# Performance work log

Hardware: AMD Instinct MI355X
Metric: run time of the kernel (lower is better)

The kernel has to match this reference:

```python
import jax, jax.numpy as jnp
import numpy as np

DELTA = -5.0
DECAY = 0.95
EPS = 1e-05


def setup_inputs() -> dict:
    key = jax.random.key(0)
    k1, k2, k3 = jax.random.split(key, 3)
    N, K, D = 16384, 1024, 256
    z = jax.random.normal(k1, (N, D), dtype=jnp.float32)
    centroids = jax.random.normal(k2, (K, D), dtype=jnp.float32)
    ema_w = jax.random.normal(k3, (K, D), dtype=jnp.float32)
    ema_cluster_size = jnp.ones((K,), dtype=jnp.float32)
    return {"z": z, "centroids": centroids, "ema_w": ema_w,
            "ema_cluster_size": ema_cluster_size}


def reference(z, centroids, ema_w, ema_cluster_size):
    # z: [N, D]; centroids/ema_w: [K, D]; ema_cluster_size: [K]
    K = centroids.shape[0]
    # squared L2 distances via ||z||^2 - 2 z.C^T + ||c||^2 (same math as
    # sum((z[:,None,:]-C)**2, -1), without the (N,K,D) intermediate)
    z_sq = jnp.sum(z * z, axis=1, keepdims=True)          # [N, 1]
    c_sq = jnp.sum(centroids * centroids, axis=1)         # [K]
    z_dist = z_sq - 2.0 * (z @ centroids.T) + c_sq        # [N, K]
    gamma = jax.nn.softmax(DELTA * z_dist, axis=1)        # [N, K]
    idx = jnp.argmax(gamma, axis=1)                       # [N] int
    # recons = one_hot(idx) @ centroids == gather
    recons = centroids[idx]                               # [N, D]
    # --- EMA codebook update (training branch), expressed purely ---
    counts = jnp.zeros((K,), dtype=z.dtype).at[idx].add(jnp.ones((), z.dtype))
    new_cs = ema_cluster_size * DECAY + (1.0 - DECAY) * counts
    n = jnp.sum(new_cs)
    new_cs = (new_cs + EPS) / (n + K * EPS) * n
    dw = jax.ops.segment_sum(z, idx, num_segments=K)      # == Idx.T @ z, [K, D]
    new_w = ema_w * DECAY + (1.0 - DECAY) * dw
    new_centroids = new_w / new_cs[:, None]
    # straight-through estimator
    recons = z + jax.lax.stop_gradient(recons - z)
    return recons, gamma, new_centroids
```

## Files before the change

### kernel.cpp

```cpp
#include <hip/hip_runtime.h>


#define DECAY 0.95f
#define OMD   0.05f
#define EPSV  1e-5f

using i32x4  = __attribute__((ext_vector_type(4))) int;
using i32x16 = __attribute__((ext_vector_type(16))) int;

typedef __attribute__((address_space(3))) unsigned int       lds_uint;
typedef const __attribute__((address_space(1))) unsigned int glb_uint;

__device__ __forceinline__ void gload16(const void* g, const void* l) {
  __builtin_amdgcn_global_load_lds((glb_uint*)(unsigned long long)g,
                                   (lds_uint*)(unsigned int)(unsigned long long)l,
                                   16, 0, 0);
}

__global__ __launch_bounds__(256) void prep(const float* __restrict__ z,
                                            const float* __restrict__ cent,
                                            const float* __restrict__ ema_cs,
                                            signed char* __restrict__ z8,
                                            signed char* __restrict__ c8,
                                            float* __restrict__ sz,
                                            float* __restrict__ sc,
                                            float* __restrict__ csq,
                                            float* __restrict__ S) {
  const int bid = blockIdx.x;
  const int t   = threadIdx.x;
  if (bid < 2176) {
    const bool isz = bid < 2048;
    const float* src = isz ? z : cent;
    const int rb = isz ? bid : (bid - 2048);
    const int r  = rb * 8 + (t >> 5);
    const int d0 = (t & 31) * 8;
    const float4 a = *(const float4*)&src[(size_t)r * 256 + d0];
    const float4 b = *(const float4*)&src[(size_t)r * 256 + d0 + 4];
    float f[8] = {a.x, a.y, a.z, a.w, b.x, b.y, b.z, b.w};
    float am = 0.f, ssq = 0.f;
#pragma unroll
    for (int j = 0; j < 8; ++j) { am = fmaxf(am, fabsf(f[j])); ssq += f[j] * f[j]; }
#pragma unroll
    for (int off = 16; off; off >>= 1) {
      am  = fmaxf(am, __shfl_down(am, off, 32));
      ssq += __shfl_down(ssq, off, 32);
    }
    am = __shfl(am, 0, 32);
    const float s  = fmaxf(am, 1e-6f) * (1.0f / 127.0f);
    const float rs = 1.0f / s;
    union { signed char c[8]; uint2 u; } H, L;
#pragma unroll
    for (int j = 0; j < 8; ++j) {
      float q = rintf(f[j] * rs);
      q = fminf(fmaxf(q, -127.f), 127.f);
      H.c[j] = (signed char)(int)q;
      float res = f[j] - q * s;
      float lq = rintf(res * rs * 256.0f);
      lq = fminf(fmaxf(lq, -127.f), 127.f);
      L.c[j] = (signed char)(int)lq;
    }
    signed char* dst = (isz ? z8 : c8) + (size_t)r * 512 + (d0 >> 6) * 128 + (d0 & 63);
    *(uint2*)dst        = H.u;
    *(uint2*)(dst + 64) = L.u;
    if ((t & 31) == 0) {
      if (isz) sz[r] = s;
      else { sc[r] = s; csq[r] = ssq; }
    }
  } else {
    float s = ema_cs[t] + ema_cs[t + 256] + ema_cs[t + 512] + ema_cs[t + 768];
#pragma unroll
    for (int off = 32; off; off >>= 1) s += __shfl_down(s, off);
    __shared__ float wsum[4];
    if ((t & 63) == 0) wsum[t >> 6] = s;
    __syncthreads();
    if (t == 0) S[0] = wsum[0] + wsum[1] + wsum[2] + wsum[3];
  }
}

__global__ __launch_bounds__(256, 2) void dist_gemm_i8(
    const signed char* __restrict__ z8, const signed char* __restrict__ c8,
    const float* __restrict__ sz, const float* __restrict__ sc,
    const float* __restrict__ csq, float* __restrict__ dist) {
  __shared__ signed char lds[2][128 * 128];

  const int tid  = threadIdx.x;
  const int lane = tid & 63;
  const int w    = tid >> 6;

  const int bid = blockIdx.x;
  const int lin = (bid & 7) * 128 + (bid >> 3);
  const int m0  = (lin >> 3) * 128;
  const int n0  = (lin & 7) * 128;

  const int wm0 = (w >> 1) * 64;
  const int wn0 = (w & 1) * 64;

  i32x16 accA[2][2];
  i32x16 accB[2][2];
#pragma unroll
  for (int i = 0; i < 2; ++i)
#pragma unroll
    for (int j = 0; j < 2; ++j) {
      accA[i][j] = (i32x16)(0);
      accB[i][j] = (i32x16)(0);
    }

  const int srow = lane >> 3;
  const int scb  = lane & 7;

  for (int kk = 0; kk < 4; ++kk) {
    __syncthreads();
#pragma unroll
    for (int j = 0; j < 4; ++j) {
      const int r0    = w * 32 + j * 8;
      const int row   = r0 + srow;
      const int chunk = scb ^ (row & 7);
      gload16(z8 + (size_t)(m0 + row) * 512 + kk * 128 + chunk * 16, &lds[0][r0 * 128]);
      gload16(c8 + (size_t)(n0 + row) * 512 + kk * 128 + chunk * 16, &lds[1][r0 * 128]);
    }
    __syncthreads();
#pragma unroll
    for (int s = 0; s < 2; ++s) {
      i32x4 ah[2], al[2], bh[2], bl[2];
      const int kc = s * 2 + (lane >> 5);
#pragma unroll
      for (int fi = 0; fi < 2; ++fi) {
        const int ra = wm0 + fi * 32 + (lane & 31);
        ah[fi] = *(const i32x4*)&lds[0][ra * 128 + ((kc)     ^ (ra & 7)) * 16];
        al[fi] = *(const i32x4*)&lds[0][ra * 128 + ((kc + 4) ^ (ra & 7)) * 16];
        const int rb = wn0 + fi * 32 + (lane & 31);
        bh[fi] = *(const i32x4*)&lds[1][rb * 128 + ((kc)     ^ (rb & 7)) * 16];
        bl[fi] = *(const i32x4*)&lds[1][rb * 128 + ((kc + 4) ^ (rb & 7)) * 16];
      }
#pragma unroll
      for (int i = 0; i < 2; ++i)
#pragma unroll
        for (int j = 0; j < 2; ++j) {
          accA[i][j] = __builtin_amdgcn_mfma_i32_32x32x32_i8(ah[i], bh[j], accA[i][j], 0, 0, 0);
          accB[i][j] = __builtin_amdgcn_mfma_i32_32x32x32_i8(ah[i], bl[j], accB[i][j], 0, 0, 0);
          accB[i][j] = __builtin_amdgcn_mfma_i32_32x32x32_i8(al[i], bh[j], accB[i][j], 0, 0, 0);
        }
    }
  }

#pragma unroll
  for (int j = 0; j < 2; ++j) {
    const int colb = n0 + wn0 + j * 32 + (lane & 31);
    const float scv = sc[colb];
    const float cqv = csq[colb];
#pragma unroll
    for (int i = 0; i < 2; ++i) {
#pragma unroll
      for (int reg = 0; reg < 16; ++reg) {
        const int row = m0 + wm0 + i * 32 + (reg & 3) + 8 * (reg >> 2) + 4 * (lane >> 5);
        const float dotv = (float)accA[i][j][reg] + (float)accB[i][j][reg] * (1.0f / 256.0f);
        dist[(size_t)row * 1024 + colb] = cqv - 2.0f * sz[row] * scv * dotv;
      }
    }
  }
}

__global__ __launch_bounds__(256) void row_softmax(float* __restrict__ gamma,
                                                   int* __restrict__ fIdx,
                                                   int K) {
  const int n = blockIdx.x;
  const int t = threadIdx.x;
  float* row = gamma + (size_t)n * K;
  const float4 s = ((const float4*)row)[t];

  float mv = s.x; int mi = 4 * t;
  if (s.y < mv) { mv = s.y; mi = 4 * t + 1; }
  if (s.z < mv) { mv = s.z; mi = 4 * t + 2; }
  if (s.w < mv) { mv = s.w; mi = 4 * t + 3; }

#pragma unroll
  for (int off = 32; off; off >>= 1) {
    const float ov = __shfl_down(mv, off);
    const int   oi = __shfl_down(mi, off);
    if (ov < mv || (ov == mv && oi < mi)) { mv = ov; mi = oi; }
  }

  __shared__ float wv[4];
  __shared__ int   wi[4];
  __shared__ float fmin_s;
  __shared__ float fsum_s;
  const int wave = t >> 6;
  if ((t & 63) == 0) { wv[wave] = mv; wi[wave] = mi; }
  __syncthreads();
  if (t == 0) {
    float bv = wv[0]; int bi = wi[0];
#pragma unroll
    for (int wq = 1; wq < 4; ++wq)
      if (wv[wq] < bv || (wv[wq] == bv && wi[wq] < bi)) { bv = wv[wq]; bi = wi[wq]; }
    fmin_s = bv; fIdx[n] = bi;
  }
  __syncthreads();

  const float bm = fmin_s;
  const float e0 = __expf(-5.0f * (s.x - bm));
  const float e1 = __expf(-5.0f * (s.y - bm));
  const float e2 = __expf(-5.0f * (s.z - bm));
  const float e3 = __expf(-5.0f * (s.w - bm));
  float ls = e0 + e1 + e2 + e3;
#pragma unroll
  for (int off = 32; off; off >>= 1) ls += __shfl_down(ls, off);
  if ((t & 63) == 0) wv[wave] = ls;
  __syncthreads();
  if (t == 0) fsum_s = wv[0] + wv[1] + wv[2] + wv[3];
  __syncthreads();

  const float inv = 1.0f / fsum_s;
  float4 g;
  g.x = e0 * inv; g.y = e1 * inv; g.z = e2 * inv; g.w = e3 * inv;
  ((float4*)row)[t] = g;
}

__global__ __launch_bounds__(512) void dw_scan(const float* __restrict__ z,
                                               const int* __restrict__ fIdx,
                                               float* __restrict__ dwp,
                                               int* __restrict__ cntp) {
  __shared__ float part[8][256];
  __shared__ int scnt[8];
  const int k    = blockIdx.x >> 2;
  const int s    = blockIdx.x & 3;
  const int ww   = threadIdx.x >> 6;
  const int lane = threadIdx.x & 63;

  float4 acc0 = {0.f, 0.f, 0.f, 0.f};
  float4 acc1 = {0.f, 0.f, 0.f, 0.f};
  int cnt = 0;
  const int base = s * 4096 + ww * 512;
  for (int c = 0; c < 512; c += 256) {
    const int4 fi = *(const int4*)&fIdx[base + c + lane * 4];
    unsigned long long m[4];
    m[0] = __ballot(fi.x == k);
    m[1] = __ballot(fi.y == k);
    m[2] = __ballot(fi.z == k);
    m[3] = __ballot(fi.w == k);
    cnt += __popcll(m[0]) + __popcll(m[1]) + __popcll(m[2]) + __popcll(m[3]);
#pragma unroll
    for (int q = 0; q < 4; q += 2) {
      unsigned long long ma = m[q], mb = m[q + 1];
      while (ma | mb) {
        if (ma) {
          const int b = __builtin_ctzll(ma); ma &= ma - 1;
          const int rr = base + c + b * 4 + q;
          const float4 zv = *(const float4*)&z[(size_t)rr * 256 + lane * 4];
          acc0.x += zv.x; acc0.y += zv.y; acc0.z += zv.z; acc0.w += zv.w;
        }
        if (mb) {
          const int b = __builtin_ctzll(mb); mb &= mb - 1;
          const int rr = base + c + b * 4 + q + 1;
          const float4 zv = *(const float4*)&z[(size_t)rr * 256 + lane * 4];
          acc1.x += zv.x; acc1.y += zv.y; acc1.z += zv.z; acc1.w += zv.w;
        }
      }
    }
  }
  acc0.x += acc1.x; acc0.y += acc1.y; acc0.z += acc1.z; acc0.w += acc1.w;
  *(float4*)&part[ww][lane * 4] = acc0;
  if (lane == 0) scnt[ww] = cnt;
  __syncthreads();
  if (ww == 0) {
    float4 tot = {0.f, 0.f, 0.f, 0.f};
    int c = 0;
#pragma unroll
    for (int e = 0; e < 8; ++e) {
      const float4 p = *(const float4*)&part[e][lane * 4];
      tot.x += p.x; tot.y += p.y; tot.z += p.z; tot.w += p.w;
      c += scnt[e];
    }
    *(float4*)&dwp[(size_t)blockIdx.x * 256 + lane * 4] = tot;
    if (lane == 0) cntp[blockIdx.x] = c;
  }
}

__global__ __launch_bounds__(256) void reduce_fin(const float* __restrict__ dwp,
                                                  const int* __restrict__ cntp,
                                                  const float* __restrict__ ema_w,
                                                  const float* __restrict__ ema_cs,
                                                  const float* __restrict__ S,
                                                  float* __restrict__ outc,
                                                  float fN) {
  const int k = blockIdx.x;
  const int t = threadIdx.x;
  const size_t b0 = (size_t)k * 4 * 256 + t;
  const float dsum = (dwp[b0] + dwp[b0 + 256]) + (dwp[b0 + 512] + dwp[b0 + 768]);
  const int   c    = (cntp[k * 4] + cntp[k * 4 + 1]) + (cntp[k * 4 + 2] + cntp[k * 4 + 3]);
  const float n   = DECAY * S[0] + OMD * fN;
  const float v   = DECAY * ema_cs[k] + OMD * (float)c;
  const float ncs = (v + EPSV) / (n + 1024.0f * EPSV) * n;
  const size_t i  = (size_t)k * 256 + t;
  outc[i] = (DECAY * ema_w[i] + OMD * dsum) / ncs;
}

__global__ __launch_bounds__(256) void recons_fill(const float* __restrict__ cent,
                                                   const int* __restrict__ fIdx,
                                                   float* __restrict__ recons) {
  const int r    = blockIdx.x * 4 + (threadIdx.x >> 6);
  const int lane = threadIdx.x & 63;
  const int idx  = fIdx[r];
  *(float4*)&recons[(size_t)r * 256 + lane * 4] =
      *(const float4*)&cent[(size_t)idx * 256 + lane * 4];
}

extern "C" void kernel_launch(void* const* d_in, const int* in_sizes, int n_in,
                              void* d_out, int out_size, void* d_ws, size_t ws_size,
                              hipStream_t stream) {
  const float* z      = (const float*)d_in[0];
  const float* cent   = (const float*)d_in[1];
  const float* ema_w  = (const float*)d_in[2];
  const float* ema_cs = (const float*)d_in[3];

  const int K = in_sizes[3];
  const int D = in_sizes[1] / K;
  const int N = in_sizes[0] / D;

  float* out    = (float*)d_out;
  float* recons = out;
  float* gamma  = out + (size_t)N * D;
  float* outc   = gamma + (size_t)N * K;

  signed char* z8 = (signed char*)recons;
  float* dwp  = (float*)((char*)recons + ((size_t)8 << 20));
  int*   cntp = (int*)((char*)recons + ((size_t)12 << 20));

  signed char* c8 = (signed char*)outc;
  float* sz = (float*)((char*)outc + (size_t)K * 512);
  float* sc = sz + N;

  float* csq  = (float*)d_ws;
  float* S    = csq + K;
  int*   fIdx = (int*)(S + 1);

  prep<<<2177, 256, 0, stream>>>(z, cent, ema_cs, z8, c8, sz, sc, csq, S);

  dist_gemm_i8<<<(N / 128) * (K / 128), 256, 0, stream>>>(z8, c8, sz, sc, csq, gamma);

  row_softmax<<<N, 256, 0, stream>>>(gamma, fIdx, K);

  dw_scan<<<K * 4, 512, 0, stream>>>(z, fIdx, dwp, cntp);

  reduce_fin<<<K, 256, 0, stream>>>(dwp, cntp, ema_w, ema_cs, S, outc, (float)N);

  recons_fill<<<N / 4, 256, 0, stream>>>(cent, fIdx, recons);
}
```

Baseline: 81.33 us.

## Fuse softmax into GEMM via two-pass recompute with per-tile row stats

Replaces the distance GEMM plus separate row softmax with a first GEMM pass that emits per-column-tile row min, argmin and exp-sums. A small merge kernel combines these into the final max, inverse sum and index. A second GEMM pass then recomputes distances and writes normalized gamma directly. This removes the write and re-read of the full distance matrix, at the cost of running the int8 GEMM twice.

```diff
diff --git a/kernel.cpp b/kernel.cpp
--- a/kernel.cpp
+++ b/kernel.cpp
@@ -77,15 +77,17 @@
   }
 }
 
-__global__ __launch_bounds__(256, 2) void dist_gemm_i8(
+__global__ __launch_bounds__(256, 2) void gemm_stats(
     const signed char* __restrict__ z8, const signed char* __restrict__ c8,
     const float* __restrict__ sz, const float* __restrict__ sc,
-    const float* __restrict__ csq, float* __restrict__ dist) {
+    const float* __restrict__ csq,
+    float* __restrict__ sm, float* __restrict__ se, int* __restrict__ si) {
   __shared__ signed char lds[2][128 * 128];
 
   const int tid  = threadIdx.x;
   const int lane = tid & 63;
   const int w    = tid >> 6;
+  const int hi   = lane >> 5, l31 = lane & 31;
 
   const int bid = blockIdx.x;
   const int lin = (bid & 7) * 128 + (bid >> 3);
@@ -94,16 +96,13 @@
 
   const int wm0 = (w >> 1) * 64;
   const int wn0 = (w & 1) * 64;
-
-  i32x16 accA[2][2];
-  i32x16 accB[2][2];
+  const int wc  = w & 1;
+
+  i32x16 accA[2][2], accB[2][2];
 #pragma unroll
   for (int i = 0; i < 2; ++i)
 #pragma unroll
-    for (int j = 0; j < 2; ++j) {
-      accA[i][j] = (i32x16)(0);
-      accB[i][j] = (i32x16)(0);
-    }
+    for (int j = 0; j < 2; ++j) { accA[i][j] = (i32x16)(0); accB[i][j] = (i32x16)(0); }
 
   const int srow = lane >> 3;
   const int scb  = lane & 7;
@@ -122,13 +121,13 @@
 #pragma unroll
     for (int s = 0; s < 2; ++s) {
       i32x4 ah[2], al[2], bh[2], bl[2];
-      const int kc = s * 2 + (lane >> 5);
+      const int kc = s * 2 + hi;
 #pragma unroll
       for (int fi = 0; fi < 2; ++fi) {
-        const int ra = wm0 + fi * 32 + (lane & 31);
+        const int ra = wm0 + fi * 32 + l31;
         ah[fi] = *(const i32x4*)&lds[0][ra * 128 + ((kc)     ^ (ra & 7)) * 16];
         al[fi] = *(const i32x4*)&lds[0][ra * 128 + ((kc + 4) ^ (ra & 7)) * 16];
-        const int rb = wn0 + fi * 32 + (lane & 31);
+        const int rb = wn0 + fi * 32 + l31;
         bh[fi] = *(const i32x4*)&lds[1][rb * 128 + ((kc)     ^ (rb & 7)) * 16];
         bl[fi] = *(const i32x4*)&lds[1][rb * 128 + ((kc + 4) ^ (rb & 7)) * 16];
       }
@@ -143,76 +142,149 @@
     }
   }
 
-#pragma unroll
-  for (int j = 0; j < 2; ++j) {
-    const int colb = n0 + wn0 + j * 32 + (lane & 31);
-    const float scv = sc[colb];
-    const float cqv = csq[colb];
-#pragma unroll
-    for (int i = 0; i < 2; ++i) {
-#pragma unroll
-      for (int reg = 0; reg < 16; ++reg) {
-        const int row = m0 + wm0 + i * 32 + (reg & 3) + 8 * (reg >> 2) + 4 * (lane >> 5);
-        const float dotv = (float)accA[i][j][reg] + (float)accB[i][j][reg] * (1.0f / 256.0f);
-        dist[(size_t)row * 1024 + colb] = cqv - 2.0f * sz[row] * scv * dotv;
+  const int colb = n0 + wn0 + l31;
+  const float sc0 = sc[colb],      cq0 = csq[colb];
+  const float sc1 = sc[colb + 32], cq1 = csq[colb + 32];
+  const int cb16 = (lin & 7) * 2 + wc;
+
+#pragma unroll
+  for (int i = 0; i < 2; ++i) {
+#pragma unroll
+    for (int reg = 0; reg < 16; ++reg) {
+      const int lr = wm0 + i * 32 + (reg & 3) + 8 * (reg >> 2) + 4 * hi;
+      const float szr = sz[m0 + lr];
+      const float d0 = (float)accA[i][0][reg] + (float)accB[i][0][reg] * (1.0f / 256.0f);
+      const float d1 = (float)accA[i][1][reg] + (float)accB[i][1][reg] * (1.0f / 256.0f);
+      const float s0 = cq0 - 2.0f * szr * sc0 * d0;
+      const float s1 = cq1 - 2.0f * szr * sc1 * d1;
+      float mv; int mi;
+      if (s1 < s0) { mv = s1; mi = colb + 32; } else { mv = s0; mi = colb; }
+#pragma unroll
+      for (int off = 16; off; off >>= 1) {
+        const float ov = __shfl_xor(mv, off);
+        const int   oi = __shfl_xor(mi, off);
+        if (ov < mv || (ov == mv && oi < mi)) { mv = ov; mi = oi; }
       }
-    }
-  }
-}
-
-__global__ __launch_bounds__(256) void row_softmax(float* __restrict__ gamma,
-                                                   int* __restrict__ fIdx,
-                                                   int K) {
-  const int n = blockIdx.x;
-  const int t = threadIdx.x;
-  float* row = gamma + (size_t)n * K;
-  const float4 s = ((const float4*)row)[t];
-
-  float mv = s.x; int mi = 4 * t;
-  if (s.y < mv) { mv = s.y; mi = 4 * t + 1; }
-  if (s.z < mv) { mv = s.z; mi = 4 * t + 2; }
-  if (s.w < mv) { mv = s.w; mi = 4 * t + 3; }
-
-#pragma unroll
-  for (int off = 32; off; off >>= 1) {
-    const float ov = __shfl_down(mv, off);
-    const int   oi = __shfl_down(mi, off);
-    if (ov < mv || (ov == mv && oi < mi)) { mv = ov; mi = oi; }
-  }
-
-  __shared__ float wv[4];
-  __shared__ int   wi[4];
-  __shared__ float fmin_s;
-  __shared__ float fsum_s;
-  const int wave = t >> 6;
-  if ((t & 63) == 0) { wv[wave] = mv; wi[wave] = mi; }
-  __syncthreads();
-  if (t == 0) {
-    float bv = wv[0]; int bi = wi[0];
-#pragma unroll
-    for (int wq = 1; wq < 4; ++wq)
-      if (wv[wq] < bv || (wv[wq] == bv && wi[wq] < bi)) { bv = wv[wq]; bi = wi[wq]; }
-    fmin_s = bv; fIdx[n] = bi;
-  }
-  __syncthreads();
-
-  const float bm = fmin_s;
-  const float e0 = __expf(-5.0f * (s.x - bm));
-  const float e1 = __expf(-5.0f * (s.y - bm));
-  const float e2 = __expf(-5.0f * (s.z - bm));
-  const float e3 = __expf(-5.0f * (s.w - bm));
-  float ls = e0 + e1 + e2 + e3;
-#pragma unroll
-  for (int off = 32; off; off >>= 1) ls += __shfl_down(ls, off);
-  if ((t & 63) == 0) wv[wave] = ls;
-  __syncthreads();
-  if (t == 0) fsum_s = wv[0] + wv[1] + wv[2] + wv[3];
-  __syncthreads();
-
-  const float inv = 1.0f / fsum_s;
-  float4 g;
-  g.x = e0 * inv; g.y = e1 * inv; g.z = e2 * inv; g.w = e3 * inv;
-  ((float4*)row)[t] = g;
+      float e = __expf(-5.0f * (s0 - mv)) + __expf(-5.0f * (s1 - mv));
+#pragma unroll
+      for (int off = 16; off; off >>= 1) e += __shfl_xor(e, off);
+      if (l31 == 0) {
+        const int gr = cb16 * 16384 + m0 + lr;
+        sm[gr] = mv; se[gr] = e; si[gr] = mi;
+      }
+    }
+  }
+}
+
+__global__ __launch_bounds__(256, 2) void gemm_gamma(
+    const signed char* __restrict__ z8, const signed char* __restrict__ c8,
+    const float* __restrict__ sz, const float* __restrict__ sc,
+    const float* __restrict__ csq,
+    const float* __restrict__ fM, const float* __restrict__ fInv,
+    float* __restrict__ gamma) {
+  __shared__ signed char lds[2][128 * 128];
+  __shared__ float fMl[128], fIl[128];
+
+  const int tid  = threadIdx.x;
+  const int lane = tid & 63;
+  const int w    = tid >> 6;
+  const int hi   = lane >> 5, l31 = lane & 31;
+
+  const int bid = blockIdx.x;
+  const int lin = (bid & 7) * 128 + (bid >> 3);
+  const int m0  = (lin >> 3) * 128;
+  const int n0  = (lin & 7) * 128;
+
+  const int wm0 = (w >> 1) * 64;
+  const int wn0 = (w & 1) * 64;
+
+  if (tid < 128) { fMl[tid] = fM[m0 + tid]; fIl[tid] = fInv[m0 + tid]; }
+
+  i32x16 accA[2][2], accB[2][2];
+#pragma unroll
+  for (int i = 0; i < 2; ++i)
+#pragma unroll
+    for (int j = 0; j < 2; ++j) { accA[i][j] = (i32x16)(0); accB[i][j] = (i32x16)(0); }
+
+  const int srow = lane >> 3;
+  const int scb  = lane & 7;
+
+  for (int kk = 0; kk < 4; ++kk) {
+    __syncthreads();
+#pragma unroll
+    for (int j = 0; j < 4; ++j) {
+      const int r0    = w * 32 + j * 8;
+      const int row   = r0 + srow;
+      const int chunk = scb ^ (row & 7);
+      gload16(z8 + (size_t)(m0 + row) * 512 + kk * 128 + chunk * 16, &lds[0][r0 * 128]);
+      gload16(c8 + (size_t)(n0 + row) * 512 + kk * 128 + chunk * 16, &lds[1][r0 * 128]);
+    }
+    __syncthreads();
+#pragma unroll
+    for (int s = 0; s < 2; ++s) {
+      i32x4 ah[2], al[2], bh[2], bl[2];
+      const int kc = s * 2 + hi;
+#pragma unroll
+      for (int fi = 0; fi < 2; ++fi) {
+        const int ra = wm0 + fi * 32 + l31;
+        ah[fi] = *(const i32x4*)&lds[0][ra * 128 + ((kc)     ^ (ra & 7)) * 16];
+        al[fi] = *(const i32x4*)&lds[0][ra * 128 + ((kc + 4) ^ (ra & 7)) * 16];
+        const int rb = wn0 + fi * 32 + l31;
+        bh[fi] = *(const i32x4*)&lds[1][rb * 128 + ((kc)     ^ (rb & 7)) * 16];
+        bl[fi] = *(const i32x4*)&lds[1][rb * 128 + ((kc + 4) ^ (rb & 7)) * 16];
+      }
+#pragma unroll
+      for (int i = 0; i < 2; ++i)
+#pragma unroll
+        for (int j = 0; j < 2; ++j) {
+          accA[i][j] = __builtin_amdgcn_mfma_i32_32x32x32_i8(ah[i], bh[j], accA[i][j], 0, 0, 0);
+          accB[i][j] = __builtin_amdgcn_mfma_i32_32x32x32_i8(ah[i], bl[j], accB[i][j], 0, 0, 0);
+          accB[i][j] = __builtin_amdgcn_mfma_i32_32x32x32_i8(al[i], bh[j], accB[i][j], 0, 0, 0);
+        }
+    }
+  }
+
+  const int colb = n0 + wn0 + l31;
+  const float sc0 = sc[colb],      cq0 = csq[colb];
+  const float sc1 = sc[colb + 32], cq1 = csq[colb + 32];
+
+#pragma unroll
+  for (int i = 0; i < 2; ++i) {
+#pragma unroll
+    for (int reg = 0; reg < 16; ++reg) {
+      const int lr = wm0 + i * 32 + (reg & 3) + 8 * (reg >> 2) + 4 * hi;
+      const float szr = sz[m0 + lr];
+      const float d0 = (float)accA[i][0][reg] + (float)accB[i][0][reg] * (1.0f / 256.0f);
+      const float d1 = (float)accA[i][1][reg] + (float)accB[i][1][reg] * (1.0f / 256.0f);
+      const float s0 = cq0 - 2.0f * szr * sc0 * d0;
+      const float s1 = cq1 - 2.0f * szr * sc1 * d1;
+      const float m = fMl[lr], inv = fIl[lr];
+      float* gp = &gamma[(size_t)(m0 + lr) * 1024];
+      gp[colb]      = __expf(-5.0f * (s0 - m)) * inv;
+      gp[colb + 32] = __expf(-5.0f * (s1 - m)) * inv;
+    }
+  }
+}
+
+__global__ __launch_bounds__(256) void merge_stats(const float* __restrict__ sm,
+                                                   const float* __restrict__ se,
+                                                   const int* __restrict__ si,
+                                                   float* __restrict__ fM,
+                                                   float* __restrict__ fInv,
+                                                   int* __restrict__ fIdx) {
+  const int r = blockIdx.x * 256 + threadIdx.x;
+  float m = sm[r]; int mi = si[r];
+#pragma unroll
+  for (int cb = 1; cb < 16; ++cb) {
+    const float mt = sm[cb * 16384 + r];
+    const int   it = si[cb * 16384 + r];
+    if (mt < m || (mt == m && it < mi)) { m = mt; mi = it; }
+  }
+  float sum = 0.f;
+#pragma unroll
+  for (int cb = 0; cb < 16; ++cb)
+    sum += se[cb * 16384 + r] * __expf(-5.0f * (sm[cb * 16384 + r] - m));
+  fM[r] = m; fInv[r] = 1.0f / sum; fIdx[r] = mi;
 }
 
 __global__ __launch_bounds__(512) void dw_scan(const float* __restrict__ z,
@@ -322,8 +394,11 @@
   float* outc   = gamma + (size_t)N * K;
 
   signed char* z8 = (signed char*)recons;
-  float* dwp  = (float*)((char*)recons + ((size_t)8 << 20));
-  int*   cntp = (int*)((char*)recons + ((size_t)12 << 20));
+  float* sm  = (float*)((char*)recons + ((size_t)8 << 20));
+  float* se  = (float*)((char*)recons + ((size_t)9 << 20));
+  int*   si  = (int*)  ((char*)recons + ((size_t)10 << 20));
+  float* dwp = (float*)((char*)recons + ((size_t)11 << 20));
+  int*  cntp = (int*)  ((char*)recons + ((size_t)15 << 20));
 
   signed char* c8 = (signed char*)outc;
   float* sz = (float*)((char*)outc + (size_t)K * 512);
@@ -331,13 +406,17 @@
 
   float* csq  = (float*)d_ws;
   float* S    = csq + K;
-  int*   fIdx = (int*)(S + 1);
+  float* fM   = S + 1;
+  float* fInv = fM + N;
+  int*   fIdx = (int*)(fInv + N);
 
   prep<<<2177, 256, 0, stream>>>(z, cent, ema_cs, z8, c8, sz, sc, csq, S);
 
-  dist_gemm_i8<<<(N / 128) * (K / 128), 256, 0, stream>>>(z8, c8, sz, sc, csq, gamma);
-
-  row_softmax<<<N, 256, 0, stream>>>(gamma, fIdx, K);
+  gemm_stats<<<(N / 128) * (K / 128), 256, 0, stream>>>(z8, c8, sz, sc, csq, sm, se, si);
+
+  merge_stats<<<N / 256, 256, 0, stream>>>(sm, se, si, fM, fInv, fIdx);
+
+  gemm_gamma<<<(N / 128) * (K / 128), 256, 0, stream>>>(z8, c8, sz, sc, csq, fM, fInv, gamma);
 
   dw_scan<<<K * 4, 512, 0, stream>>>(z, fIdx, dwp, cntp);
 
```

Result: slower. 126.1 us (+55.1%).
